# Kernel optimization log

Measured on AMD Instinct MI355X. Metric: run time of the kernel, lower is better.

Reference implementation:

```python
import jax, jax.numpy as jnp
import numpy as np

EPS = 1e-5


def _bn(x, g, b):
    # BatchNorm1d in training mode: batch mean, biased variance, eps=1e-5
    m = jnp.mean(x, axis=0)
    v = jnp.var(x, axis=0)
    return (x - m) * jax.lax.rsqrt(v + EPS) * g + b


def setup_inputs() -> dict:
    key = jax.random.key(0)
    ks = jax.random.split(key, 16)
    B, N, F, H = 4096, 128, 4, 32
    w = lambda k, o, i: jax.random.normal(k, (o, i), jnp.float32) * 0.3
    d = {
        'u': jax.random.normal(ks[0], (B, N, F), jnp.float32),
        'mask': jnp.ones((B * N, 1), jnp.int32),
        # MLPphi params
        'p_bn1_g': jnp.ones((F,), jnp.float32), 'p_bn1_b': jnp.zeros((F,), jnp.float32), 'p_w1': w(ks[1], H, F),
        'p_bn2_g': jnp.ones((H,), jnp.float32), 'p_bn2_b': jnp.zeros((H,), jnp.float32), 'p_w2': w(ks[2], H, H),
        'p_bn3_g': jnp.ones((H,), jnp.float32), 'p_bn3_b': jnp.zeros((H,), jnp.float32), 'p_w3': w(ks[3], H, H),
        # MLPomega params
        'o_bn1_g': jnp.ones((F,), jnp.float32), 'o_bn1_b': jnp.zeros((F,), jnp.float32), 'o_w1': w(ks[4], H, F),
        'o_bn2_g': jnp.ones((H,), jnp.float32), 'o_bn2_b': jnp.zeros((H,), jnp.float32), 'o_w2': w(ks[5], H, H),
        'o_bn3_g': jnp.ones((H,), jnp.float32), 'o_bn3_b': jnp.zeros((H,), jnp.float32), 'o_w3': w(ks[6], H, H),
        # MLPtheta params
        't_bn1_g': jnp.ones((H,), jnp.float32), 't_bn1_b': jnp.zeros((H,), jnp.float32), 't_w1': w(ks[7], H, H),
        't_bn2_g': jnp.ones((H,), jnp.float32), 't_bn2_b': jnp.zeros((H,), jnp.float32), 't_w2': w(ks[8], H, H),
        't_bn3_g': jnp.ones((H,), jnp.float32), 't_bn3_b': jnp.zeros((H,), jnp.float32), 't_w3': w(ks[9], H, H),
        't_bn4_g': jnp.ones((H,), jnp.float32), 't_bn4_b': jnp.zeros((H,), jnp.float32),
        't_w4': w(ks[10], 1, H), 't_b4': jnp.zeros((1,), jnp.float32),
    }
    return d


def _forward(u, mask,
             p_bn1_g, p_bn1_b, p_w1, p_bn2_g, p_bn2_b, p_w2, p_bn3_g, p_bn3_b, p_w3,
             o_bn1_g, o_bn1_b, o_w1, o_bn2_g, o_bn2_b, o_w2, o_bn3_g, o_bn3_b, o_w3,
             t_bn1_g, t_bn1_b, t_w1, t_bn2_g, t_bn2_b, t_w2, t_bn3_g, t_bn3_b, t_w3,
             t_bn4_g, t_bn4_b, t_w4, t_b4):
    B, N, F = u.shape
    H = p_w1.shape[0]
    u_flat = u.reshape(-1, F)  # (B*N, F)

    # MLPphi: three BN+Linear(no bias)+Tanh blocks with residual adds (dropout=identity in eval)
    o1 = jnp.tanh(_bn(u_flat, p_bn1_g, p_bn1_b) @ p_w1.T)
    o2 = jnp.tanh(_bn(o1, p_bn2_g, p_bn2_b) @ p_w2.T)
    o3 = jnp.tanh(_bn(o1 + o2, p_bn3_g, p_bn3_b) @ p_w3.T)
    x_main = (o1 + o2 + o3).reshape(B, N, H)

    # MLPomega: BN+Linear+Tanh x2, BN+Linear, softmax over hidden dim (dim=1 of flat), then masked_fill
    a = jnp.tanh(_bn(u_flat, o_bn1_g, o_bn1_b) @ o_w1.T)
    a = jnp.tanh(_bn(a, o_bn2_g, o_bn2_b) @ o_w2.T)
    a = _bn(a, o_bn3_g, o_bn3_b) @ o_w3.T
    a = jax.nn.softmax(a, axis=1)
    a = jnp.where(mask == 0, -jnp.inf, a)
    x_attn = a.reshape(B, N, H)

    # attention pooling over neighbors
    x = jnp.sum(x_main * x_attn, axis=1)  # (B, H)

    x = jnp.tanh(_bn(x, t_bn1_g, t_bn1_b) @ t_w1.T)
    x = jnp.tanh(_bn(x, t_bn2_g, t_bn2_b) @ t_w2.T)
    x = jnp.tanh(_bn(x, t_bn3_g, t_bn3_b) @ t_w3.T)
    x = _bn(x, t_bn4_g, t_bn4_b) @ t_w4.T + t_b4
    return x


def reference(u, mask,
              p_bn1_g, p_bn1_b, p_w1, p_bn2_g, p_bn2_b, p_w2, p_bn3_g, p_bn3_b, p_w3,
              o_bn1_g, o_bn1_b, o_w1, o_bn2_g, o_bn2_b, o_w2, o_bn3_g, o_bn3_b, o_w3,
              t_bn1_g, t_bn1_b, t_w1, t_bn2_g, t_bn2_b, t_w2, t_bn3_g, t_bn3_b, t_w3,
              t_bn4_g, t_bn4_b, t_w4, t_b4):
    return _forward(u, mask,
                    p_bn1_g, p_bn1_b, p_w1, p_bn2_g, p_bn2_b, p_w2, p_bn3_g, p_bn3_b, p_w3,
                    o_bn1_g, o_bn1_b, o_w1, o_bn2_g, o_bn2_b, o_w2, o_bn3_g, o_bn3_b, o_w3,
                    t_bn1_g, t_bn1_b, t_w1, t_bn2_g, t_bn2_b, t_w2, t_bn3_g, t_bn3_b, t_w3,
                    t_bn4_g, t_bn4_b, t_w4, t_b4)
```

## Files before the change

### kernel.cpp

```cpp
#include <hip/hip_runtime.h>

typedef unsigned int u32;
typedef unsigned short u16;
typedef __attribute__((ext_vector_type(8))) _Float16 half8;
typedef __attribute__((ext_vector_type(4))) float f32x4;

#define ROWS  524288
#define BROWS 4096
#define EPS   1e-5f

#define S_U   0
#define S_O1  8
#define S_A1  72
#define S_O12 136
#define S_A2  200
#define S_X   264
#define S_X1  328
#define S_X2  392
#define S_X3  456
#define SHARD 1024
#define NSH   64

#define XSTR 40

// ... 195 lines not shown

#define KIND_TANH          0
#define KIND_TANHRES       2
#define KIND_TANHRES_ATREG 3
template<int KIND>
__device__ __forceinline__ void mfma_layer(u16* X, const u16* Wt, const float* Cb,
                                           int L, int wv, int lane, const u32* at_pk)
{
  int ln15 = lane & 15, quad = lane >> 4;
  half8 w0 = *(const half8*)&Wt[(L*32 + ln15     )*XSTR + quad*8];
  half8 w1 = *(const half8*)&Wt[(L*32 + ln15 + 16)*XSTR + quad*8];
  float bias0[4], bias1[4];
#pragma unroll
  for (int reg=0;reg<4;++reg){
    bias0[reg] = Cb[L*32 +      quad*4 + reg];
    bias1[reg] = Cb[L*32 + 16 + quad*4 + reg];
  }
  int rowbase = wv*64;
#pragma unroll
  for (int Mt=0; Mt<4; ++Mt){
    int s = rowbase + Mt*16 + ln15;
    half8 bfr = *(const half8*)&X[s*XSTR + quad*8];
    f32x4 c0 = {0.f,0.f,0.f,0.f}, c1 = {0.f,0.f,0.f,0.f};
    c0 = __builtin_amdgcn_mfma_f32_16x16x32_f16(w0, bfr, c0, 0,0,0);
    c1 = __builtin_amdgcn_mfma_f32_16x16x32_f16(w1, bfr, c1, 0,0,0);
    float o0[4], o1v[4];
    if (KIND == KIND_TANHRES || KIND == KIND_TANHRES_ATREG){
      unpk4(*(const uint2*)&X[s*XSTR +      quad*4], o0);
      unpk4(*(const uint2*)&X[s*XSTR + 16 + quad*4], o1v);
    }
    float a0v[4], a1v[4];
    if (KIND == KIND_TANHRES_ATREG){
      a0v[0]=lo16(at_pk[Mt*4+0]); a0v[1]=hi16(at_pk[Mt*4+0]);
      a0v[2]=lo16(at_pk[Mt*4+1]); a0v[3]=hi16(at_pk[Mt*4+1]);
      a1v[0]=lo16(at_pk[Mt*4+2]); a1v[1]=hi16(at_pk[Mt*4+2]);
      a1v[2]=lo16(at_pk[Mt*4+3]); a1v[3]=hi16(at_pk[Mt*4+3]);
    }
    float v0[4], v1[4];
#pragma unroll
    for (int reg=0;reg<4;++reg){
      float a = c0[reg] + bias0[reg];
      float b = c1[reg] + bias1[reg];
      if (KIND == KIND_TANH){ a = tanh_fast(a); b = tanh_fast(b); }
      else if (KIND == KIND_TANHRES){ a = o0[reg] + tanh_fast(a); b = o1v[reg] + tanh_fast(b); }
      else if (KIND == KIND_TANHRES_ATREG){
        a = (o0[reg] + tanh_fast(a)) * a0v[reg];
        b = (o1v[reg] + tanh_fast(b)) * a1v[reg];
      }
      v0[reg] = a; v1[reg] = b;
    }
    uint2 w0o, w1o;
    w0o.x = pack2h(v0[0], v0[1]); w0o.y = pack2h(v0[2], v0[3]);
    w1o.x = pack2h(v1[0], v1[1]); w1o.y = pack2h(v1[2], v1[3]);
    *(uint2*)&X[s*XSTR +      quad*4] = w0o;
    *(uint2*)&X[s*XSTR + 16 + quad*4] = w1o;
  }
}

__device__ __forceinline__ void emit_stats(float* s8, float* q8, int tid, int wv,
    int quad, int ln15, float* scr , float* __restrict__ S, int offS, int shard)
{
#pragma unroll
  for (int i=0;i<8;++i){ s8[i]=red16(s8[i]); q8[i]=red16(q8[i]); }
  __syncthreads();
  if (ln15 == 0){
#pragma unroll
    for (int rg=0; rg<4; ++rg){
      int cl = quad*4+rg, ch = 16+quad*4+rg;
      scr[wv*64 + cl]       = s8[rg];
      scr[wv*64 + ch]       = s8[4+rg];
      scr[256 + wv*64 + cl] = q8[rg];
      scr[256 + wv*64 + ch] = q8[4+rg];
    }
  }
  __syncthreads();
  if (tid < 64){
    int j = tid & 31, isq = tid >> 5;
    const float* src = scr + isq*256;
    float tot = src[j] + src[64+j] + src[128+j] + src[192+j];
    atomicAdd(&S[shard*SHARD + offS + isq*32 + j], tot);
  }
}

__device__ __forceinline__ void mfma_logits_softmax_r(const half8* fa,
    const u16* Wt, const float* Cb, int L, int lane,
    const int* __restrict__ mask, int maskbase, u32* at_pk)
{
  int ln15 = lane & 15, quad = lane >> 4;
  half8 w0 = *(const half8*)&Wt[(L*32 + ln15     )*XSTR + quad*8];
  half8 w1 = *(const half8*)&Wt[(L*32 + ln15 + 16)*XSTR + quad*8];
  float bias0[4], bias1[4];
#pragma unroll
  for (int reg=0;reg<4;++reg){
    bias0[reg] = Cb[L*32 +      quad*4 + reg];
    bias1[reg] = Cb[L*32 + 16 + quad*4 + reg];
  }
#pragma unroll
  for (int Mt=0; Mt<4; ++Mt){
    f32x4 c0 = {0.f,0.f,0.f,0.f}, c1 = {0.f,0.f,0.f,0.f};
    c0 = __builtin_amdgcn_mfma_f32_16x16x32_f16(w0, fa[Mt], c0, 0,0,0);
    c1 = __builtin_amdgcn_mfma_f32_16x16x32_f16(w1, fa[Mt], c1, 0,0,0);
    float l0[4], l1[4];
#pragma unroll
    for (int reg=0;reg<4;++reg){ l0[reg] = c0[reg]+bias0[reg]; l1[reg] = c1[reg]+bias1[reg]; }
    float mx = l0[0];
#pragma unroll
    for (int reg=1;reg<4;++reg) mx = fmaxf(mx, l0[reg]);
#pragma unroll
    for (int reg=0;reg<4;++reg) mx = fmaxf(mx, l1[reg]);
    mx = fmaxf(mx, __shfl_xor(mx, 16));
    mx = fmaxf(mx, __shfl_xor(mx, 32));
    float sum = 0.f;
#pragma unroll
    for (int reg=0;reg<4;++reg){ l0[reg] = __expf(l0[reg]-mx); sum += l0[reg]; }
#pragma unroll
    for (int reg=0;reg<4;++reg){ l1[reg] = __expf(l1[reg]-mx); sum += l1[reg]; }
    sum += __shfl_xor(sum, 16);
    sum += __shfl_xor(sum, 32);
    float inv = __builtin_amdgcn_rcpf(sum);
    bool mz = (mask[maskbase + Mt*16 + ln15] == 0);
#pragma unroll
    for (int reg=0;reg<4;++reg){
      l0[reg] *= inv; l1[reg] *= inv;
      if (mz){ l0[reg] = -__builtin_inff(); l1[reg] = -__builtin_inff(); }
    }
    at_pk[Mt*4+0] = pack2h(l0[0], l0[1]);
    at_pk[Mt*4+1] = pack2h(l0[2], l0[3]);
    at_pk[Mt*4+2] = pack2h(l1[0], l1[1]);
    at_pk[Mt*4+3] = pack2h(l1[2], l1[3]);
  }
}

__device__ __forceinline__ void mfma_pool_r(const half8* fo, const uint2* r0, const uint2* r1,
    const u16* Wt, const float* Cb, int L, int lane, const u32* at_pk, float* ps)
{
  int ln15 = lane & 15, quad = lane >> 4;
  half8 w0 = *(const half8*)&Wt[(L*32 + ln15     )*XSTR + quad*8];
  half8 w1 = *(const half8*)&Wt[(L*32 + ln15 + 16)*XSTR + quad*8];
  float bias0[4], bias1[4];
#pragma unroll
  for (int reg=0;reg<4;++reg){
    bias0[reg] = Cb[L*32 +      quad*4 + reg];
    bias1[reg] = Cb[L*32 + 16 + quad*4 + reg];
  }
#pragma unroll
  for (int i=0;i<8;++i) ps[i]=0.f;
#pragma unroll
  for (int Mt=0; Mt<4; ++Mt){
    f32x4 c0 = {0.f,0.f,0.f,0.f}, c1 = {0.f,0.f,0.f,0.f};
    c0 = __builtin_amdgcn_mfma_f32_16x16x32_f16(w0, fo[Mt], c0, 0,0,0);
    c1 = __builtin_amdgcn_mfma_f32_16x16x32_f16(w1, fo[Mt], c1, 0,0,0);
    float o0[4], o1v[4];
    unpk4(r0[Mt], o0); unpk4(r1[Mt], o1v);
    float a0v[4], a1v[4];
    a0v[0]=lo16(at_pk[Mt*4+0]); a0v[1]=hi16(at_pk[Mt*4+0]);
    a0v[2]=lo16(at_pk[Mt*4+1]); a0v[3]=hi16(at_pk[Mt*4+1]);
    a1v[0]=lo16(at_pk[Mt*4+2]); a1v[1]=hi16(at_pk[Mt*4+2]);
    a1v[2]=lo16(at_pk[Mt*4+3]); a1v[3]=hi16(at_pk[Mt*4+3]);
#pragma unroll
    for (int reg=0;reg<4;++reg){
      float a = (o0[reg]  + tanh_fast(c0[reg]+bias0[reg])) * a0v[reg];
      float b = (o1v[reg] + tanh_fast(c1[reg]+bias1[reg])) * a1v[reg];
      ps[reg]   += a;
      ps[4+reg] += b;
    }
  }
}

__device__ __forceinline__ void reduce_f16(const u16* X, float* lds2,
                                           float* __restrict__ S, int offS, int shard)
{
  int tid = threadIdx.x;
  __syncthreads();
  {
    int j = tid & 31, seg = tid >> 5;
    float s=0.f, q=0.f;
#pragma unroll
    for (int q2=0;q2<32;++q2){
      float v = h2f(X[(seg*32+q2)*XSTR + j]);
      s += v; q = fmaf(v,v,q);
    }
    lds2[seg*32+j] = s;
    lds2[256 + seg*32+j] = q;
  }
  __syncthreads();
  if (tid < 64){
    int j = tid & 31; bool isq = tid >= 32;
    const float* src = lds2 + (isq?256:0);
    float tot=0.f;
#pragma unroll
    for (int sg=0;sg<8;++sg) tot += src[sg*32+j];
    atomicAdd(&S[shard*SHARD + offS + (isq?32:0) + j], tot);
  }
  __syncthreads();
}

__device__ __forceinline__ void reduce_f32(const float* Xs, float* lds2,
                                           float* __restrict__ S, int offS, int shard)
{
  int tid = threadIdx.x;
  __syncthreads();
  {
    int j = tid & 31, seg = tid >> 5;
    float s=0.f, q=0.f;
#pragma unroll
    for (int q2=0;q2<32;++q2){
      float v = Xs[(seg*32+q2)*33 + j];
      s += v; q = fmaf(v,v,q);
    }
    lds2[seg*32+j] = s;
    lds2[256 + seg*32+j] = q;
  }
  __syncthreads();
  if (tid < 64){
    int j = tid & 31; bool isq = tid >= 32;
    const float* src = lds2 + (isq?256:0);
    float tot=0.f;
#pragma unroll
    for (int sg=0;sg<8;++sg) tot += src[sg*32+j];
    atomicAdd(&S[shard*SHARD + offS + (isq?32:0) + j], tot);
  }
  __syncthreads();
}

template<bool F32, bool MAT>
__device__ __forceinline__ void pass1_body(const void* __restrict__ u,
    const void* pg1, const void* pb1, const void* pw1,
    const void* og1, const void* ob1, const void* ow1,
    float* __restrict__ S, u16* __restrict__ o1g, u16* __restrict__ a1g,
    u16* X, float* lds2, float* mr)
{
  int tid = threadIdx.x;
  int r = blockIdx.x*256 + tid;
  int shard = blockIdx.x & (NSH-1);
  float f[4], xn[4];
  load_u4<F32>(u,r,f);
  prep_u_par(S, mr, lds2, tid);

  bn_u_l<F32>(mr, pg1, pb1, f, xn);
  chain1_out<F32,MAT>(xn, pw1, X + tid*XSTR, o1g + (size_t)r*32);
  reduce_f16(X, lds2, S, S_O1, shard);

  bn_u_l<F32>(mr, og1, ob1, f, xn);
  chain1_out<F32,MAT>(xn, ow1, X + tid*XSTR, a1g + (size_t)r*32);
  reduce_f16(X, lds2, S, S_A1, shard);
}
template<bool MAT>
__global__ __launch_bounds__(256) void k_pass1(const void* __restrict__ u,
    const void* pg1, const void* pb1, const void* pw1,
    const void* og1, const void* ob1, const void* ow1,
    float* __restrict__ S, u16* o1g, u16* a1g){
  __shared__ u16 X[256*XSTR];
  __shared__ float lds2[512];
  __shared__ float mr[8];
  __shared__ int sf;
  int isf = detect_u((const u16*)u, threadIdx.x, &sf);
  if (isf) pass1_body<true ,MAT>(u,pg1,pb1,pw1,og1,ob1,ow1,S,o1g,a1g,X,lds2,mr);
  else     pass1_body<false,MAT>(u,pg1,pb1,pw1,og1,ob1,ow1,S,o1g,a1g,X,lds2,mr);
}

template<bool F32>
__device__ __forceinline__ void pass2m_body(
    const void* pg2, const void* pb2, const void* pw2,
    const void* og2, const void* ob2, const void* ow2,
    float* __restrict__ S, u16* __restrict__ o12g, u16* __restrict__ a2g,
    u16* Wt, float* Cb, float* lds2)
{
  int tid = threadIdx.x;
  int wv = tid >> 6, lane = tid & 63;
  int ln15 = lane & 15, quad = lane >> 4;
  int gbase = blockIdx.x*256;
  int shard = blockIdx.x & (NSH-1);

  half8 fo[4], fa[4]; uint2 r0[4], r1[4];
  int rowbase = wv*64;
#pragma unroll
  for (int Mt=0; Mt<4; ++Mt){
    size_t R = (size_t)(gbase + rowbase + Mt*16 + ln15);
    fo[Mt] = *(const half8*)&o12g[R*32 + quad*8];
    r0[Mt] = *(const uint2*)&o12g[R*32 +      quad*4];
    r1[Mt] = *(const uint2*)&o12g[R*32 + 16 + quad*4];
    fa[Mt] = *(const half8*)&a2g [R*32 + quad*8];
  }

  fold2<F32>(S, S_O1, S_A1, pg2,pb2,pw2, og2,ob2,ow2, Wt, Cb, lds2);

  float s8[8], q8[8];

  {
    half8 w0 = *(const half8*)&Wt[(ln15     )*XSTR + quad*8];
    half8 w1 = *(const half8*)&Wt[(ln15 + 16)*XSTR + quad*8];
    float bias0[4], bias1[4];
#pragma unroll
    for (int reg=0;reg<4;++reg){
      bias0[reg] = Cb[     quad*4 + reg];
      bias1[reg] = Cb[16 + quad*4 + reg];
    }
#pragma unroll
    for (int i=0;i<8;++i){ s8[i]=0.f; q8[i]=0.f; }
#pragma unroll
    for (int Mt=0; Mt<4; ++Mt){
      f32x4 c0 = {0.f,0.f,0.f,0.f}, c1 = {0.f,0.f,0.f,0.f};
      c0 = __builtin_amdgcn_mfma_f32_16x16x32_f16(w0, fo[Mt], c0, 0,0,0);
      c1 = __builtin_amdgcn_mfma_f32_16x16x32_f16(w1, fo[Mt], c1, 0,0,0);
      float o0[4], o1v[4];
      unpk4(r0[Mt], o0); unpk4(r1[Mt], o1v);
      float v0[4], v1[4];
#pragma unroll
      for (int reg=0;reg<4;++reg){
        float a = o0[reg]  + tanh_fast(c0[reg] + bias0[reg]);
        float b = o1v[reg] + tanh_fast(c1[reg] + bias1[reg]);
        s8[reg]   += a; q8[reg]   = fmaf(a,a,q8[reg]);
        s8[4+reg] += b; q8[4+reg] = fmaf(b,b,q8[4+reg]);
        v0[reg] = a; v1[reg] = b;
      }
      uint2 w0o, w1o;
      w0o.x = pack2h(v0[0], v0[1]); w0o.y = pack2h(v0[2], v0[3]);
      w1o.x = pack2h(v1[0], v1[1]); w1o.y = pack2h(v1[2], v1[3]);
      size_t R = (size_t)(gbase + rowbase + Mt*16 + ln15);
      *(uint2*)&o12g[R*32 +      quad*4] = w0o;
      *(uint2*)&o12g[R*32 + 16 + quad*4] = w1o;
    }
    emit_stats(s8, q8, tid, wv, quad, ln15, lds2, S, S_O12, shard);
  }

  {
    half8 w0 = *(const half8*)&Wt[(32 + ln15     )*XSTR + quad*8];
    half8 w1 = *(const half8*)&Wt[(32 + ln15 + 16)*XSTR + quad*8];
    float bias0[4], bias1[4];
#pragma unroll
    for (int reg=0;reg<4;++reg){
      bias0[reg] = Cb[32 +      quad*4 + reg];
      bias1[reg] = Cb[32 + 16 + quad*4 + reg];
    }
#pragma unroll
    for (int i=0;i<8;++i){ s8[i]=0.f; q8[i]=0.f; }
#pragma unroll
    for (int Mt=0; Mt<4; ++Mt){
      f32x4 c0 = {0.f,0.f,0.f,0.f}, c1 = {0.f,0.f,0.f,0.f};
      c0 = __builtin_amdgcn_mfma_f32_16x16x32_f16(w0, fa[Mt], c0, 0,0,0);
      c1 = __builtin_amdgcn_mfma_f32_16x16x32_f16(w1, fa[Mt], c1, 0,0,0);
      float v0[4], v1[4];
#pragma unroll
      for (int reg=0;reg<4;++reg){
        float a = tanh_fast(c0[reg] + bias0[reg]);
        float b = tanh_fast(c1[reg] + bias1[reg]);
        s8[reg]   += a; q8[reg]   = fmaf(a,a,q8[reg]);
        s8[4+reg] += b; q8[4+reg] = fmaf(b,b,q8[4+reg]);
        v0[reg] = a; v1[reg] = b;
      }
      uint2 w0o, w1o;
      w0o.x = pack2h(v0[0], v0[1]); w0o.y = pack2h(v0[2], v0[3]);
      w1o.x = pack2h(v1[0], v1[1]); w1o.y = pack2h(v1[2], v1[3]);
      size_t R = (size_t)(gbase + rowbase + Mt*16 + ln15);
      *(uint2*)&a2g[R*32 +      quad*4] = w0o;
      *(uint2*)&a2g[R*32 + 16 + quad*4] = w1o;
    }
    emit_stats(s8, q8, tid, wv, quad, ln15, lds2, S, S_A2, shard);
  }
}
__global__ __launch_bounds__(256) void k_pass2m(const void* __restrict__ u,
    const void* pg2, const void* pb2, const void* pw2,
    const void* og2, const void* ob2, const void* ow2,
    float* __restrict__ S, u16* o12g, u16* a2g){
  __shared__ u16 Wt[2*32*XSTR];
  __shared__ float Cb[64];
  __shared__ float lds2[512];
  __shared__ int sf;
  int isf = detect_u((const u16*)u, threadIdx.x, &sf);
  if (isf) pass2m_body<true >(pg2,pb2,pw2,og2,ob2,ow2,S,o12g,a2g,Wt,Cb,lds2);
  else     pass2m_body<false>(pg2,pb2,pw2,og2,ob2,ow2,S,o12g,a2g,Wt,Cb,lds2);
}

template<int KIND>
__device__ __forceinline__ void mfma_stat_l(const u16* X, const u16* Wt, const float* Cb,
    int L, int wv, int lane, float* s8, float* q8)
{
  int ln15 = lane & 15, quad = lane >> 4;
  half8 w0 = *(const half8*)&Wt[(L*32 + ln15     )*XSTR + quad*8];
  half8 w1 = *(const half8*)&Wt[(L*32 + ln15 + 16)*XSTR + quad*8];
  float bias0[4], bias1[4];
#pragma unroll
  for (int reg=0;reg<4;++reg){
    bias0[reg] = Cb[L*32 +      quad*4 + reg];
    bias1[reg] = Cb[L*32 + 16 + quad*4 + reg];
  }
#pragma unroll
  for (int i=0;i<8;++i){ s8[i]=0.f; q8[i]=0.f; }
  int rowbase = wv*64;
#pragma unroll
  for (int Mt=0; Mt<4; ++Mt){
    int s = rowbase + Mt*16 + ln15;
    half8 bfr = *(const half8*)&X[s*XSTR + quad*8];
    f32x4 c0 = {0.f,0.f,0.f,0.f}, c1 = {0.f,0.f,0.f,0.f};
    c0 = __builtin_amdgcn_mfma_f32_16x16x32_f16(w0, bfr, c0, 0,0,0);
    c1 = __builtin_amdgcn_mfma_f32_16x16x32_f16(w1, bfr, c1, 0,0,0);
    float o0[4], o1v[4];
    if (KIND == KIND_TANHRES){
      unpk4(*(const uint2*)&X[s*XSTR +      quad*4], o0);
      unpk4(*(const uint2*)&X[s*XSTR + 16 + quad*4], o1v);
    }
#pragma unroll
    for (int reg=0;reg<4;++reg){
      float a = c0[reg] + bias0[reg];
      float b = c1[reg] + bias1[reg];
      if (KIND == KIND_TANH){ a = tanh_fast(a); b = tanh_fast(b); }
      else { a = o0[reg] + tanh_fast(a); b = o1v[reg] + tanh_fast(b); }
      s8[reg]   += a; q8[reg]   = fmaf(a,a,q8[reg]);
      s8[4+reg] += b; q8[4+reg] = fmaf(b,b,q8[4+reg]);
    }
  }
}
template<bool F32>
__device__ __forceinline__ void pass2_body(const void* __restrict__ u,
    const void* pg1, const void* pb1, const void* pw1,
    const void* og1, const void* ob1, const void* ow1,
    const void* pg2, const void* pb2, const void* pw2,
    const void* og2, const void* ob2, const void* ow2,
    float* __restrict__ S,
    u16* X, u16* Wt, float* Cb, float* lds2, float* mr)
{
  int tid = threadIdx.x;
  int wv = tid >> 6, lane = tid & 63;
  int ln15 = lane & 15, quad = lane >> 4;
  int r = blockIdx.x*256 + tid;
  int shard = blockIdx.x & (NSH-1);
  float f[4], xn[4];
  load_u4<F32>(u,r,f);
  prep_u_par(S, mr, lds2, tid);
  fold2<F32>(S, S_O1, S_A1, pg2,pb2,pw2, og2,ob2,ow2, Wt, Cb, lds2);

  float s8[8], q8[8];

  bn_u_l<F32>(mr, pg1, pb1, f, xn);
  chain1_out<F32,false>(xn, pw1, X + tid*XSTR, 0);
  __syncthreads();
  mfma_stat_l<KIND_TANHRES>(X, Wt, Cb, 0, wv, lane, s8, q8);
  emit_stats(s8, q8, tid, wv, quad, ln15, lds2, S, S_O12, shard);

  bn_u_l<F32>(mr, og1, ob1, f, xn);
  chain1_out<F32,false>(xn, ow1, X + tid*XSTR, 0);
  __syncthreads();
  mfma_stat_l<KIND_TANH>(X, Wt, Cb, 1, wv, lane, s8, q8);
  emit_stats(s8, q8, tid, wv, quad, ln15, lds2, S, S_A2, shard);
}
__global__ __launch_bounds__(256) void k_pass2(const void* __restrict__ u,
    const void* pg1, const void* pb1, const void* pw1,
    const void* og1, const void* ob1, const void* ow1,
    const void* pg2, const void* pb2, const void* pw2,
    const void* og2, const void* ob2, const void* ow2,
    float* __restrict__ S){
  __shared__ u16 X[256*XSTR];
  __shared__ u16 Wt[2*32*XSTR];
  __shared__ float Cb[64];
  __shared__ float lds2[512];
  __shared__ float mr[8];
  __shared__ int sf;
  int isf = detect_u((const u16*)u, threadIdx.x, &sf);
  if (isf) pass2_body<true >(u,pg1,pb1,pw1,og1,ob1,ow1,pg2,pb2,pw2,og2,ob2,ow2,S,X,Wt,Cb,lds2,mr);
  else     pass2_body<false>(u,pg1,pb1,pw1,og1,ob1,ow1,pg2,pb2,pw2,og2,ob2,ow2,S,X,Wt,Cb,lds2,mr);
}

template<bool F32>
__device__ __forceinline__ void pass3m_body(const int* __restrict__ mask,
    const void* pg3, const void* pb3, const void* pw3,
    const void* og3, const void* ob3, const void* ow3,
    const u16* __restrict__ o12g, const u16* __restrict__ a2g,
    float* __restrict__ x, float* __restrict__ S,
    u16* Wt, float* Cb, float* lds2)
{
  int tid = threadIdx.x;
  int wv = tid >> 6, lane = tid & 63;
  int ln15 = lane & 15, quad = lane >> 4;
  int gbase = blockIdx.x*256;
  int rowbase = wv*64;

  half8 fo[4], fa[4]; uint2 r0[4], r1[4];
#pragma unroll
  for (int Mt=0; Mt<4; ++Mt){
    size_t R = (size_t)(gbase + rowbase + Mt*16 + ln15);
    fa[Mt] = *(const half8*)&a2g [R*32 + quad*8];
    fo[Mt] = *(const half8*)&o12g[R*32 + quad*8];
    r0[Mt] = *(const uint2*)&o12g[R*32 +      quad*4];
    r1[Mt] = *(const uint2*)&o12g[R*32 + 16 + quad*4];
  }

  fold2<F32>(S, S_A2, S_O12, og3,ob3,ow3, pg3,pb3,pw3, Wt, Cb, lds2);

  u32 at_pk[16];
  int maskbase = gbase + wv*64;
  mfma_logits_softmax_r(fa, Wt, Cb, 0, lane, mask, maskbase, at_pk);

  float ps[8];
  mfma_pool_r(fo, r0, r1, Wt, Cb, 1, lane, at_pk, ps);

#pragma unroll
  for (int i=0;i<8;++i) ps[i]=red16(ps[i]);
  __syncthreads();
  if (ln15 == 0){
#pragma unroll
    for (int rg=0; rg<4; ++rg){
      lds2[wv*32 + quad*4+rg]    = ps[rg];
      lds2[wv*32 + 16+quad*4+rg] = ps[4+rg];
    }
  }
  __syncthreads();
  if (tid < 64){
    int half = tid >> 5, j = tid & 31;
    float v = lds2[half*64 + j] + lds2[half*64 + 32 + j];
    x[(blockIdx.x*2 + half)*32 + j] = v;
    float* Sh = S + (blockIdx.x & (NSH-1))*SHARD;
    atomicAdd(&Sh[S_X+j], v);
    atomicAdd(&Sh[S_X+32+j], v*v);
  }
}
__global__ __launch_bounds__(256) void k_pass3m(const void* __restrict__ u, const int* __restrict__ mask,
    const void* pg3, const void* pb3, const void* pw3,
    const void* og3, const void* ob3, const void* ow3,
    const u16* o12g, const u16* a2g,
    float* __restrict__ x, float* __restrict__ S){
  __shared__ u16 Wt[2*32*XSTR];
  __shared__ float Cb[64];
  __shared__ float lds2[512];
  __shared__ int sf;
  int isf = detect_u((const u16*)u, threadIdx.x, &sf);
  if (isf) pass3m_body<true >(mask,pg3,pb3,pw3,og3,ob3,ow3,o12g,a2g,x,S,Wt,Cb,lds2);
  else     pass3m_body<false>(mask,pg3,pb3,pw3,og3,ob3,ow3,o12g,a2g,x,S,Wt,Cb,lds2);
}

template<bool F32>
__device__ __forceinline__ void fold4(const float* __restrict__ S,
    int off0,int off1,int off2,int off3,
    const void* g0,const void* b0,const void* W0,
    const void* g1,const void* b1,const void* W1,
    const void* g2,const void* b2,const void* W2,
    const void* g3,const void* b3,const void* W3,
    u16* Wt, float* Cb, float* scr)
{
  int tid = threadIdx.x;
  __shared__ float scr2[256];
  if (tid < 128){
    int L = tid>>5, k = tid&31;
    const void* g = (L==0)?g0:(L==1)?g1:(L==2)?g2:g3;
    const void* b = (L==0)?b0:(L==1)?b1:(L==2)?b2:b3;
    int off = (L==0)?off0:(L==1)?off1:(L==2)?off2:off3;
    float s=0.f, q=0.f;
#pragma unroll
    for (int sh=0; sh<NSH; ++sh){
      s += S[sh*SHARD + off + k];
      q += S[sh*SHARD + off + 32 + k];
    }
    float m    = s*(1.0f/ROWS);
    float var  = q*(1.0f/ROWS) - m*m;
    float rstd = rsqrtf(var+EPS);
    float sc = rdp<F32>(g,k)*rstd;
    scr[tid]  = sc;
    scr2[tid] = rdp<F32>(b,k) - m*sc;
  }
  __syncthreads();
  if (tid < 128){
    int L = tid>>5, j = tid&31;
    const void* W = (L==0)?W0:(L==1)?W1:(L==2)?W2:W3;
    float c = 0.f;
#pragma unroll
    for (int k=0;k<32;++k){
      float Wv = rdp<F32>(W, j*32+k);
      Wt[(L*32+j)*XSTR + k] = f2h(Wv * scr[(L<<5)|k]);
      c += Wv * scr2[(L<<5)|k];
    }
    Cb[L*32+j] = c;
  }
  __syncthreads();
}

template<bool F32>
__device__ __forceinline__ void pass3_body(const void* __restrict__ u, const int* __restrict__ mask,
    const void* pg1, const void* pb1, const void* pw1,
    const void* og1, const void* ob1, const void* ow1,
    const void* pg2, const void* pb2, const void* pw2,
    const void* og2, const void* ob2, const void* ow2,
    const void* pg3, const void* pb3, const void* pw3,
    const void* og3, const void* ob3, const void* ow3,
    float* __restrict__ x, float* __restrict__ S,
    u16* X, u16* Wt, float* Cb, float* red2, float* mr)
{
  int tid = threadIdx.x;
  int wv = tid >> 6, lane = tid & 63;
  int r = blockIdx.x*256 + tid;
  float f[4], xn[4];
  load_u4<F32>(u,r,f);
  prep_u_par(S, mr, red2, tid);
  fold4<F32>(S, S_A1, S_A2, S_O1, S_O12,
             og2,ob2,ow2, og3,ob3,ow3, pg2,pb2,pw2, pg3,pb3,pw3,
             Wt, Cb, red2);

  u32 at_pk[16];
// ... 163 lines not shown
    const float* __restrict__ xin, float* __restrict__ xout,
    float* __restrict__ S, int off_in, int off_out,
    const void* g, const void* b, const void* W){
  __shared__ float lds[256*33];
  __shared__ float lds2[512];
  __shared__ int sf;
  int isf = detect_u((const u16*)u, threadIdx.x, &sf);
  if (isf) theta_L_body<true , NSH_IN>(xin, xout, S, off_in, off_out, g, b, W, lds, lds2);
  else     theta_L_body<false, NSH_IN>(xin, xout, S, off_in, off_out, g, b, W, lds, lds2);
}

template<bool F32>
__device__ __forceinline__ void theta_fin_body(const float* __restrict__ xin,
    float* __restrict__ S,
    const void* g4, const void* b4, const void* w4, const void* bb4,
    void* out, float* lds, float* lds2)
{
  int tid = threadIdx.x, blk = blockIdx.x;
  int r = blk*256 + tid;
  const float4* xr = (const float4*)&xin[(size_t)r*32];
  float4 t0 = xr[0], t1 = xr[1], t2 = xr[2], t3 = xr[3];
  float4 t4 = xr[4], t5 = xr[5], t6 = xr[6], t7 = xr[7];
  theta_gather<16>(S, S_X3, lds, lds2, tid);
  float vv[32];
  vv[0]=t0.x; vv[1]=t0.y; vv[2]=t0.z; vv[3]=t0.w;
  vv[4]=t1.x; vv[5]=t1.y; vv[6]=t1.z; vv[7]=t1.w;
  vv[8]=t2.x; vv[9]=t2.y; vv[10]=t2.z; vv[11]=t2.w;
  vv[12]=t3.x; vv[13]=t3.y; vv[14]=t3.z; vv[15]=t3.w;
  vv[16]=t4.x; vv[17]=t4.y; vv[18]=t4.z; vv[19]=t4.w;
  vv[20]=t5.x; vv[21]=t5.y; vv[22]=t5.z; vv[23]=t5.w;
  vv[24]=t6.x; vv[25]=t6.y; vv[26]=t6.z; vv[27]=t6.w;
  vv[28]=t7.x; vv[29]=t7.y; vv[30]=t7.z; vv[31]=t7.w;
  float acc = rdp<F32>(bb4, 0);
#pragma unroll
  for (int k=0;k<32;++k){
    float xnv = (vv[k] - lds2[k]) * (rdp<F32>(g4,k)*lds2[32+k]) + rdp<F32>(b4,k);
    acc = fmaf(rdp<F32>(w4,k), xnv, acc);
  }
  if (F32) ((float*)out)[r] = acc;
  else     ((u16*)out)[r]  = f2b(acc);
}
__global__ __launch_bounds__(256) void k_theta_fin(const void* __restrict__ u,
    const float* __restrict__ xin, float* __restrict__ S,
    const void* g4, const void* b4, const void* w4, const void* bb4,
    void* out){
  __shared__ float lds[256];
  __shared__ float lds2[512];
  __shared__ int sf;
  int isf = detect_u((const u16*)u, threadIdx.x, &sf);
  if (isf) theta_fin_body<true >(xin, S, g4, b4, w4, bb4, out, lds, lds2);
  else     theta_fin_body<false>(xin, S, g4, b4, w4, bb4, out, lds, lds2);
}

extern "C" void kernel_launch(void* const* d_in, const int* in_sizes, int n_in,
                              void* d_out, int out_size, void* d_ws, size_t ws_size,
                              hipStream_t stream)
{
  const void* u    = d_in[0];
  const int*  mask = (const int*)d_in[1];
  const void *pg1=d_in[2],  *pb1=d_in[3],  *pw1=d_in[4];
  const void *pg2=d_in[5],  *pb2=d_in[6],  *pw2=d_in[7];
  const void *pg3=d_in[8],  *pb3=d_in[9],  *pw3=d_in[10];
  const void *og1=d_in[11], *ob1=d_in[12], *ow1=d_in[13];
  const void *og2=d_in[14], *ob2=d_in[15], *ow2=d_in[16];
  const void *og3=d_in[17], *ob3=d_in[18], *ow3=d_in[19];
  const void *tg1=d_in[20], *tb1=d_in[21], *tw1=d_in[22];
  const void *tg2=d_in[23], *tb2=d_in[24], *tw2=d_in[25];
  const void *tg3=d_in[26], *tb3=d_in[27], *tw3=d_in[28];
  const void *tg4=d_in[29], *tb4=d_in[30], *tw4=d_in[31], *tbb4=d_in[32];

  char* ws = (char*)d_ws;
  float* S    = (float*)(ws + 4096);
  float* x    = (float*)(ws + 524288);
  float* xb   = (float*)(ws + 1048576);

  const size_t MB = 1024*1024;
  u16* o12g = (u16*)(ws + 8*MB);
  u16* a2g  = (u16*)(ws + 40*MB);
  bool MAT = ws_size >= 73*MB;

  (void)hipMemsetAsync(ws, 0, 4096 + NSH*SHARD*4, stream);
  k_stats_u<<<1024, 256, 0, stream>>>(u, S);
  if (MAT){
    k_pass1<true ><<<2048, 256, 0, stream>>>(u, pg1,pb1,pw1, og1,ob1,ow1, S, o12g, a2g);
    k_pass2m<<<2048, 256, 0, stream>>>(u, pg2,pb2,pw2, og2,ob2,ow2, S, o12g, a2g);
    k_pass3m<<<2048, 256, 0, stream>>>(u, mask, pg3,pb3,pw3, og3,ob3,ow3, o12g, a2g, x, S);
  } else {
    k_pass1<false><<<2048, 256, 0, stream>>>(u, pg1,pb1,pw1, og1,ob1,ow1, S, o12g, a2g);
    k_pass2<<<2048, 256, 0, stream>>>(u, pg1,pb1,pw1, og1,ob1,ow1,
                                      pg2,pb2,pw2, og2,ob2,ow2, S);
    k_pass3<<<2048, 256, 0, stream>>>(u, mask, pg1,pb1,pw1, og1,ob1,ow1,
                                      pg2,pb2,pw2, og2,ob2,ow2,
                                      pg3,pb3,pw3, og3,ob3,ow3, x, S);
  }
  k_theta_L<64><<<16, 256, 0, stream>>>(u, x,  xb, S, S_X,  S_X1, tg1, tb1, tw1);
  k_theta_L<16><<<16, 256, 0, stream>>>(u, xb, x,  S, S_X1, S_X2, tg2, tb2, tw2);
  k_theta_L<16><<<16, 256, 0, stream>>>(u, x,  xb, S, S_X2, S_X3, tg3, tb3, tw3);
  k_theta_fin<<<16, 256, 0, stream>>>(u, xb, S, tg4, tb4, tw4, tbb4, d_out);
}
```

Baseline: 330.2 us.

## Process four row tiles per block with double-buffered loads in passes

The three main passes now launch a quarter of the blocks, and each block loops over four 256-row groups. Passes 2m and 3m double-buffer the half8 MFMA operand loads, prefetching the next group while computing the current one. The per-block fold of BN statistics into weights and the weight and bias register loads are amortised over four times as many rows, and BN stat emission in pass 2 happens once per block. The trade-offs are higher register pressure from the doubled buffers and only 512 blocks, which may reduce occupancy and latency hiding.

```diff
diff --git a/kernel.cpp b/kernel.cpp
--- a/kernel.cpp
+++ b/kernel.cpp
@@ -301,91 +301,6 @@
   }
 }
 
-__device__ __forceinline__ void mfma_logits_softmax_r(const half8* fa,
-    const u16* Wt, const float* Cb, int L, int lane,
-    const int* __restrict__ mask, int maskbase, u32* at_pk)
-{
-  int ln15 = lane & 15, quad = lane >> 4;
-  half8 w0 = *(const half8*)&Wt[(L*32 + ln15     )*XSTR + quad*8];
-  half8 w1 = *(const half8*)&Wt[(L*32 + ln15 + 16)*XSTR + quad*8];
-  float bias0[4], bias1[4];
-#pragma unroll
-  for (int reg=0;reg<4;++reg){
-    bias0[reg] = Cb[L*32 +      quad*4 + reg];
-    bias1[reg] = Cb[L*32 + 16 + quad*4 + reg];
-  }
-#pragma unroll
-  for (int Mt=0; Mt<4; ++Mt){
-    f32x4 c0 = {0.f,0.f,0.f,0.f}, c1 = {0.f,0.f,0.f,0.f};
-    c0 = __builtin_amdgcn_mfma_f32_16x16x32_f16(w0, fa[Mt], c0, 0,0,0);
-    c1 = __builtin_amdgcn_mfma_f32_16x16x32_f16(w1, fa[Mt], c1, 0,0,0);
-    float l0[4], l1[4];
-#pragma unroll
-    for (int reg=0;reg<4;++reg){ l0[reg] = c0[reg]+bias0[reg]; l1[reg] = c1[reg]+bias1[reg]; }
-    float mx = l0[0];
-#pragma unroll
-    for (int reg=1;reg<4;++reg) mx = fmaxf(mx, l0[reg]);
-#pragma unroll
-    for (int reg=0;reg<4;++reg) mx = fmaxf(mx, l1[reg]);
-    mx = fmaxf(mx, __shfl_xor(mx, 16));
-    mx = fmaxf(mx, __shfl_xor(mx, 32));
-    float sum = 0.f;
-#pragma unroll
-    for (int reg=0;reg<4;++reg){ l0[reg] = __expf(l0[reg]-mx); sum += l0[reg]; }
-#pragma unroll
-    for (int reg=0;reg<4;++reg){ l1[reg] = __expf(l1[reg]-mx); sum += l1[reg]; }
-    sum += __shfl_xor(sum, 16);
-    sum += __shfl_xor(sum, 32);
-    float inv = __builtin_amdgcn_rcpf(sum);
-    bool mz = (mask[maskbase + Mt*16 + ln15] == 0);
-#pragma unroll
-    for (int reg=0;reg<4;++reg){
-      l0[reg] *= inv; l1[reg] *= inv;
-      if (mz){ l0[reg] = -__builtin_inff(); l1[reg] = -__builtin_inff(); }
-    }
-    at_pk[Mt*4+0] = pack2h(l0[0], l0[1]);
-    at_pk[Mt*4+1] = pack2h(l0[2], l0[3]);
-    at_pk[Mt*4+2] = pack2h(l1[0], l1[1]);
-    at_pk[Mt*4+3] = pack2h(l1[2], l1[3]);
-  }
-}
-
-__device__ __forceinline__ void mfma_pool_r(const half8* fo, const uint2* r0, const uint2* r1,
-    const u16* Wt, const float* Cb, int L, int lane, const u32* at_pk, float* ps)
-{
-  int ln15 = lane & 15, quad = lane >> 4;
-  half8 w0 = *(const half8*)&Wt[(L*32 + ln15     )*XSTR + quad*8];
-  half8 w1 = *(const half8*)&Wt[(L*32 + ln15 + 16)*XSTR + quad*8];
-  float bias0[4], bias1[4];
-#pragma unroll
-  for (int reg=0;reg<4;++reg){
-    bias0[reg] = Cb[L*32 +      quad*4 + reg];
-    bias1[reg] = Cb[L*32 + 16 + quad*4 + reg];
-  }
-#pragma unroll
-  for (int i=0;i<8;++i) ps[i]=0.f;
-#pragma unroll
-  for (int Mt=0; Mt<4; ++Mt){
-    f32x4 c0 = {0.f,0.f,0.f,0.f}, c1 = {0.f,0.f,0.f,0.f};
-    c0 = __builtin_amdgcn_mfma_f32_16x16x32_f16(w0, fo[Mt], c0, 0,0,0);
-    c1 = __builtin_amdgcn_mfma_f32_16x16x32_f16(w1, fo[Mt], c1, 0,0,0);
-    float o0[4], o1v[4];
-    unpk4(r0[Mt], o0); unpk4(r1[Mt], o1v);
-    float a0v[4], a1v[4];
-    a0v[0]=lo16(at_pk[Mt*4+0]); a0v[1]=hi16(at_pk[Mt*4+0]);
-    a0v[2]=lo16(at_pk[Mt*4+1]); a0v[3]=hi16(at_pk[Mt*4+1]);
-    a1v[0]=lo16(at_pk[Mt*4+2]); a1v[1]=hi16(at_pk[Mt*4+2]);
-    a1v[2]=lo16(at_pk[Mt*4+3]); a1v[3]=hi16(at_pk[Mt*4+3]);
-#pragma unroll
-    for (int reg=0;reg<4;++reg){
-      float a = (o0[reg]  + tanh_fast(c0[reg]+bias0[reg])) * a0v[reg];
-      float b = (o1v[reg] + tanh_fast(c1[reg]+bias1[reg])) * a1v[reg];
-      ps[reg]   += a;
-      ps[4+reg] += b;
-    }
-  }
-}
-
 __device__ __forceinline__ void reduce_f16(const u16* X, float* lds2,
                                            float* __restrict__ S, int offS, int shard)
 {
@@ -450,19 +365,25 @@
     u16* X, float* lds2, float* mr)
 {
   int tid = threadIdx.x;
-  int r = blockIdx.x*256 + tid;
+  int base = blockIdx.x*1024;
   int shard = blockIdx.x & (NSH-1);
-  float f[4], xn[4];
-  load_u4<F32>(u,r,f);
+  float f[4][4];
+#pragma unroll
+  for (int g=0; g<4; ++g) load_u4<F32>(u, base + g*256 + tid, f[g]);
   prep_u_par(S, mr, lds2, tid);
 
-  bn_u_l<F32>(mr, pg1, pb1, f, xn);
-  chain1_out<F32,MAT>(xn, pw1, X + tid*XSTR, o1g + (size_t)r*32);
-  reduce_f16(X, lds2, S, S_O1, shard);
-
-  bn_u_l<F32>(mr, og1, ob1, f, xn);
-  chain1_out<F32,MAT>(xn, ow1, X + tid*XSTR, a1g + (size_t)r*32);
-  reduce_f16(X, lds2, S, S_A1, shard);
+#pragma unroll
+  for (int g=0; g<4; ++g){
+    int r = base + g*256 + tid;
+    float xn[4];
+    bn_u_l<F32>(mr, pg1, pb1, f[g], xn);
+    chain1_out<F32,MAT>(xn, pw1, X + tid*XSTR, o1g + (size_t)r*32);
+    reduce_f16(X, lds2, S, S_O1, shard);
+
+    bn_u_l<F32>(mr, og1, ob1, f[g], xn);
+    chain1_out<F32,MAT>(xn, ow1, X + tid*XSTR, a1g + (size_t)r*32);
+    reduce_f16(X, lds2, S, S_A1, shard);
+  }
 }
 template<bool MAT>
 __global__ __launch_bounds__(256) void k_pass1(const void* __restrict__ u,
@@ -478,6 +399,12 @@
   else     pass1_body<false,MAT>(u,pg1,pb1,pw1,og1,ob1,ow1,S,o1g,a1g,X,lds2,mr);
 }
 
+#define P2_LOADM(BUF, G, MT) { \
+  size_t R = (size_t)(gbase + (G)*256 + rowbase + (MT)*16 + ln15); \
+  fo[BUF][MT] = *(const half8*)&o12g[R*32 + quad*8]; \
+  fa[BUF][MT] = *(const half8*)&a2g [R*32 + quad*8]; }
+#define P2_LOAD(BUF, G) P2_LOADM(BUF,G,0) P2_LOADM(BUF,G,1) P2_LOADM(BUF,G,2) P2_LOADM(BUF,G,3)
+
 template<bool F32>
 __device__ __forceinline__ void pass2m_body(
     const void* pg2, const void* pb2, const void* pw2,
@@ -488,95 +415,88 @@
   int tid = threadIdx.x;
   int wv = tid >> 6, lane = tid & 63;
   int ln15 = lane & 15, quad = lane >> 4;
-  int gbase = blockIdx.x*256;
+  int gbase = blockIdx.x*1024;
   int shard = blockIdx.x & (NSH-1);
-
-  half8 fo[4], fa[4]; uint2 r0[4], r1[4];
   int rowbase = wv*64;
-#pragma unroll
-  for (int Mt=0; Mt<4; ++Mt){
-    size_t R = (size_t)(gbase + rowbase + Mt*16 + ln15);
-    fo[Mt] = *(const half8*)&o12g[R*32 + quad*8];
-    r0[Mt] = *(const uint2*)&o12g[R*32 +      quad*4];
-    r1[Mt] = *(const uint2*)&o12g[R*32 + 16 + quad*4];
-    fa[Mt] = *(const half8*)&a2g [R*32 + quad*8];
-  }
+
+  half8 fo[2][4], fa[2][4];
+  P2_LOAD(0, 0)
 
   fold2<F32>(S, S_O1, S_A1, pg2,pb2,pw2, og2,ob2,ow2, Wt, Cb, lds2);
 
-  float s8[8], q8[8];
-
-  {
-    half8 w0 = *(const half8*)&Wt[(ln15     )*XSTR + quad*8];
-    half8 w1 = *(const half8*)&Wt[(ln15 + 16)*XSTR + quad*8];
-    float bias0[4], bias1[4];
-#pragma unroll
-    for (int reg=0;reg<4;++reg){
-      bias0[reg] = Cb[     quad*4 + reg];
-      bias1[reg] = Cb[16 + quad*4 + reg];
-    }
-#pragma unroll
-    for (int i=0;i<8;++i){ s8[i]=0.f; q8[i]=0.f; }
+  half8 w0o = *(const half8*)&Wt[(ln15     )*XSTR + quad*8];
+  half8 w1o = *(const half8*)&Wt[(ln15 + 16)*XSTR + quad*8];
+  half8 w0a = *(const half8*)&Wt[(32 + ln15     )*XSTR + quad*8];
+  half8 w1a = *(const half8*)&Wt[(32 + ln15 + 16)*XSTR + quad*8];
+  float b0o[4], b1o[4], b0a[4], b1a[4];
+#pragma unroll
+  for (int reg=0;reg<4;++reg){
+    b0o[reg] = Cb[     quad*4 + reg]; b1o[reg] = Cb[16 + quad*4 + reg];
+    b0a[reg] = Cb[32 + quad*4 + reg]; b1a[reg] = Cb[48 + quad*4 + reg];
+  }
+
+  float s8o[8], q8o[8], s8a[8], q8a[8];
+#pragma unroll
+  for (int i=0;i<8;++i){ s8o[i]=0.f; q8o[i]=0.f; s8a[i]=0.f; q8a[i]=0.f; }
+
+#pragma unroll
+  for (int g=0; g<4; ++g){
+    const int buf = g & 1;
+    if (g < 3){ P2_LOAD(buf^1, g+1) }
+    uint2 r0[4], r1[4];
 #pragma unroll
     for (int Mt=0; Mt<4; ++Mt){
-      f32x4 c0 = {0.f,0.f,0.f,0.f}, c1 = {0.f,0.f,0.f,0.f};
-      c0 = __builtin_amdgcn_mfma_f32_16x16x32_f16(w0, fo[Mt], c0, 0,0,0);
-      c1 = __builtin_amdgcn_mfma_f32_16x16x32_f16(w1, fo[Mt], c1, 0,0,0);
-      float o0[4], o1v[4];
-      unpk4(r0[Mt], o0); unpk4(r1[Mt], o1v);
-      float v0[4], v1[4];
-#pragma unroll
-      for (int reg=0;reg<4;++reg){
-        float a = o0[reg]  + tanh_fast(c0[reg] + bias0[reg]);
-        float b = o1v[reg] + tanh_fast(c1[reg] + bias1[reg]);
-        s8[reg]   += a; q8[reg]   = fmaf(a,a,q8[reg]);
-        s8[4+reg] += b; q8[4+reg] = fmaf(b,b,q8[4+reg]);
-        v0[reg] = a; v1[reg] = b;
+      size_t R = (size_t)(gbase + g*256 + rowbase + Mt*16 + ln15);
+      r0[Mt] = *(const uint2*)&o12g[R*32 +      quad*4];
+      r1[Mt] = *(const uint2*)&o12g[R*32 + 16 + quad*4];
+    }
+#pragma unroll
+    for (int Mt=0; Mt<4; ++Mt){
+      size_t R = (size_t)(gbase + g*256 + rowbase + Mt*16 + ln15);
+      {
+        f32x4 c0 = {0.f,0.f,0.f,0.f}, c1 = {0.f,0.f,0.f,0.f};
+        c0 = __builtin_amdgcn_mfma_f32_16x16x32_f16(w0o, fo[buf][Mt], c0, 0,0,0);
+        c1 = __builtin_amdgcn_mfma_f32_16x16x32_f16(w1o, fo[buf][Mt], c1, 0,0,0);
+        float o0[4], o1v[4];
+        unpk4(r0[Mt], o0); unpk4(r1[Mt], o1v);
+        float v0[4], v1[4];
+#pragma unroll
+        for (int reg=0;reg<4;++reg){
+          float a = o0[reg]  + tanh_fast(c0[reg] + b0o[reg]);
+          float b = o1v[reg] + tanh_fast(c1[reg] + b1o[reg]);
+          s8o[reg]   += a; q8o[reg]   = fmaf(a,a,q8o[reg]);
+          s8o[4+reg] += b; q8o[4+reg] = fmaf(b,b,q8o[4+reg]);
+          v0[reg] = a; v1[reg] = b;
+        }
+        uint2 wA, wB;
+        wA.x = pack2h(v0[0], v0[1]); wA.y = pack2h(v0[2], v0[3]);
+        wB.x = pack2h(v1[0], v1[1]); wB.y = pack2h(v1[2], v1[3]);
+        *(uint2*)&o12g[R*32 +      quad*4] = wA;
+        *(uint2*)&o12g[R*32 + 16 + quad*4] = wB;
       }
-      uint2 w0o, w1o;
-      w0o.x = pack2h(v0[0], v0[1]); w0o.y = pack2h(v0[2], v0[3]);
-      w1o.x = pack2h(v1[0], v1[1]); w1o.y = pack2h(v1[2], v1[3]);
-      size_t R = (size_t)(gbase + rowbase + Mt*16 + ln15);
-      *(uint2*)&o12g[R*32 +      quad*4] = w0o;
-      *(uint2*)&o12g[R*32 + 16 + quad*4] = w1o;
-    }
-    emit_stats(s8, q8, tid, wv, quad, ln15, lds2, S, S_O12, shard);
-  }
-
-  {
-    half8 w0 = *(const half8*)&Wt[(32 + ln15     )*XSTR + quad*8];
-    half8 w1 = *(const half8*)&Wt[(32 + ln15 + 16)*XSTR + quad*8];
-    float bias0[4], bias1[4];
-#pragma unroll
-    for (int reg=0;reg<4;++reg){
-      bias0[reg] = Cb[32 +      quad*4 + reg];
-      bias1[reg] = Cb[32 + 16 + quad*4 + reg];
-    }
-#pragma unroll
-    for (int i=0;i<8;++i){ s8[i]=0.f; q8[i]=0.f; }
-#pragma unroll
-    for (int Mt=0; Mt<4; ++Mt){
-      f32x4 c0 = {0.f,0.f,0.f,0.f}, c1 = {0.f,0.f,0.f,0.f};
-      c0 = __builtin_amdgcn_mfma_f32_16x16x32_f16(w0, fa[Mt], c0, 0,0,0);
-      c1 = __builtin_amdgcn_mfma_f32_16x16x32_f16(w1, fa[Mt], c1, 0,0,0);
-      float v0[4], v1[4];
-#pragma unroll
-      for (int reg=0;reg<4;++reg){
-        float a = tanh_fast(c0[reg] + bias0[reg]);
-        float b = tanh_fast(c1[reg] + bias1[reg]);
-        s8[reg]   += a; q8[reg]   = fmaf(a,a,q8[reg]);
-        s8[4+reg] += b; q8[4+reg] = fmaf(b,b,q8[4+reg]);
-        v0[reg] = a; v1[reg] = b;
+      {
+        f32x4 c0 = {0.f,0.f,0.f,0.f}, c1 = {0.f,0.f,0.f,0.f};
+        c0 = __builtin_amdgcn_mfma_f32_16x16x32_f16(w0a, fa[buf][Mt], c0, 0,0,0);
+        c1 = __builtin_amdgcn_mfma_f32_16x16x32_f16(w1a, fa[buf][Mt], c1, 0,0,0);
+        float v0[4], v1[4];
+#pragma unroll
+        for (int reg=0;reg<4;++reg){
+          float a = tanh_fast(c0[reg] + b0a[reg]);
+          float b = tanh_fast(c1[reg] + b1a[reg]);
+          s8a[reg]   += a; q8a[reg]   = fmaf(a,a,q8a[reg]);
+          s8a[4+reg] += b; q8a[4+reg] = fmaf(b,b,q8a[4+reg]);
+          v0[reg] = a; v1[reg] = b;
+        }
+        uint2 wA, wB;
+        wA.x = pack2h(v0[0], v0[1]); wA.y = pack2h(v0[2], v0[3]);
+        wB.x = pack2h(v1[0], v1[1]); wB.y = pack2h(v1[2], v1[3]);
+        *(uint2*)&a2g[R*32 +      quad*4] = wA;
+        *(uint2*)&a2g[R*32 + 16 + quad*4] = wB;
       }
-      uint2 w0o, w1o;
-      w0o.x = pack2h(v0[0], v0[1]); w0o.y = pack2h(v0[2], v0[3]);
-      w1o.x = pack2h(v1[0], v1[1]); w1o.y = pack2h(v1[2], v1[3]);
-      size_t R = (size_t)(gbase + rowbase + Mt*16 + ln15);
-      *(uint2*)&a2g[R*32 +      quad*4] = w0o;
-      *(uint2*)&a2g[R*32 + 16 + quad*4] = w1o;
-    }
-    emit_stats(s8, q8, tid, wv, quad, ln15, lds2, S, S_A2, shard);
-  }
+    }
+  }
+  emit_stats(s8o, q8o, tid, wv, quad, ln15, lds2, S, S_O12, shard);
+  emit_stats(s8a, q8a, tid, wv, quad, ln15, lds2, S, S_A2, shard);
 }
 __global__ __launch_bounds__(256) void k_pass2m(const void* __restrict__ u,
     const void* pg2, const void* pb2, const void* pw2,
@@ -680,6 +600,12 @@
   else     pass2_body<false>(u,pg1,pb1,pw1,og1,ob1,ow1,pg2,pb2,pw2,og2,ob2,ow2,S,X,Wt,Cb,lds2,mr);
 }
 
+#define P3_LOADM(BUF, G, MT) { \
+  size_t R = (size_t)(gbase + (G)*256 + rowbase + (MT)*16 + ln15); \
+  fa[BUF][MT] = *(const half8*)&a2g [R*32 + quad*8]; \
+  fo[BUF][MT] = *(const half8*)&o12g[R*32 + quad*8]; }
+#define P3_LOAD(BUF, G) P3_LOADM(BUF,G,0) P3_LOADM(BUF,G,1) P3_LOADM(BUF,G,2) P3_LOADM(BUF,G,3)
+
 template<bool F32>
 __device__ __forceinline__ void pass3m_body(const int* __restrict__ mask,
     const void* pg3, const void* pb3, const void* pw3,
@@ -691,46 +617,115 @@
   int tid = threadIdx.x;
   int wv = tid >> 6, lane = tid & 63;
   int ln15 = lane & 15, quad = lane >> 4;
-  int gbase = blockIdx.x*256;
+  int gbase = blockIdx.x*1024;
+  int shard = blockIdx.x & (NSH-1);
   int rowbase = wv*64;
 
-  half8 fo[4], fa[4]; uint2 r0[4], r1[4];
-#pragma unroll
-  for (int Mt=0; Mt<4; ++Mt){
-    size_t R = (size_t)(gbase + rowbase + Mt*16 + ln15);
-    fa[Mt] = *(const half8*)&a2g [R*32 + quad*8];
-    fo[Mt] = *(const half8*)&o12g[R*32 + quad*8];
-    r0[Mt] = *(const uint2*)&o12g[R*32 +      quad*4];
-    r1[Mt] = *(const uint2*)&o12g[R*32 + 16 + quad*4];
-  }
+  half8 fa[2][4], fo[2][4];
+  P3_LOAD(0, 0)
 
   fold2<F32>(S, S_A2, S_O12, og3,ob3,ow3, pg3,pb3,pw3, Wt, Cb, lds2);
 
-  u32 at_pk[16];
-  int maskbase = gbase + wv*64;
-  mfma_logits_softmax_r(fa, Wt, Cb, 0, lane, mask, maskbase, at_pk);
-
-  float ps[8];
-  mfma_pool_r(fo, r0, r1, Wt, Cb, 1, lane, at_pk, ps);
-
-#pragma unroll
-  for (int i=0;i<8;++i) ps[i]=red16(ps[i]);
-  __syncthreads();
-  if (ln15 == 0){
-#pragma unroll
-    for (int rg=0; rg<4; ++rg){
-      lds2[wv*32 + quad*4+rg]    = ps[rg];
-      lds2[wv*32 + 16+quad*4+rg] = ps[4+rg];
-    }
-  }
-  __syncthreads();
-  if (tid < 64){
-    int half = tid >> 5, j = tid & 31;
-    float v = lds2[half*64 + j] + lds2[half*64 + 32 + j];
-    x[(blockIdx.x*2 + half)*32 + j] = v;
-    float* Sh = S + (blockIdx.x & (NSH-1))*SHARD;
-    atomicAdd(&Sh[S_X+j], v);
-    atomicAdd(&Sh[S_X+32+j], v*v);
+  half8 w0s = *(const half8*)&Wt[(ln15     )*XSTR + quad*8];
+  half8 w1s = *(const half8*)&Wt[(ln15 + 16)*XSTR + quad*8];
+  half8 w0p = *(const half8*)&Wt[(32 + ln15     )*XSTR + quad*8];
+  half8 w1p = *(const half8*)&Wt[(32 + ln15 + 16)*XSTR + quad*8];
+  float b0s[4], b1s[4], b0p[4], b1p[4];
+#pragma unroll
+  for (int reg=0;reg<4;++reg){
+    b0s[reg] = Cb[     quad*4 + reg]; b1s[reg] = Cb[16 + quad*4 + reg];
+    b0p[reg] = Cb[32 + quad*4 + reg]; b1p[reg] = Cb[48 + quad*4 + reg];
+  }
+
+#pragma unroll
+  for (int g=0; g<4; ++g){
+    const int buf = g & 1;
+    if (g < 3){ P3_LOAD(buf^1, g+1) }
+    uint2 r0[4], r1[4];
+#pragma unroll
+    for (int Mt=0; Mt<4; ++Mt){
+      size_t R = (size_t)(gbase + g*256 + rowbase + Mt*16 + ln15);
+      r0[Mt] = *(const uint2*)&o12g[R*32 +      quad*4];
+      r1[Mt] = *(const uint2*)&o12g[R*32 + 16 + quad*4];
+    }
+    int maskbase = gbase + g*256 + wv*64;
+    u32 at_pk[16];
+#pragma unroll
+    for (int Mt=0; Mt<4; ++Mt){
+      f32x4 c0 = {0.f,0.f,0.f,0.f}, c1 = {0.f,0.f,0.f,0.f};
+      c0 = __builtin_amdgcn_mfma_f32_16x16x32_f16(w0s, fa[buf][Mt], c0, 0,0,0);
+      c1 = __builtin_amdgcn_mfma_f32_16x16x32_f16(w1s, fa[buf][Mt], c1, 0,0,0);
+      float l0[4], l1[4];
+#pragma unroll
+      for (int reg=0;reg<4;++reg){ l0[reg] = c0[reg]+b0s[reg]; l1[reg] = c1[reg]+b1s[reg]; }
+      float mx = l0[0];
+#pragma unroll
+      for (int reg=1;reg<4;++reg) mx = fmaxf(mx, l0[reg]);
+#pragma unroll
+      for (int reg=0;reg<4;++reg) mx = fmaxf(mx, l1[reg]);
+      mx = fmaxf(mx, __shfl_xor(mx, 16));
+      mx = fmaxf(mx, __shfl_xor(mx, 32));
+      float sum = 0.f;
+#pragma unroll
+      for (int reg=0;reg<4;++reg){ l0[reg] = __expf(l0[reg]-mx); sum += l0[reg]; }
+#pragma unroll
+      for (int reg=0;reg<4;++reg){ l1[reg] = __expf(l1[reg]-mx); sum += l1[reg]; }
+      sum += __shfl_xor(sum, 16);
+      sum += __shfl_xor(sum, 32);
+      float inv = __builtin_amdgcn_rcpf(sum);
+      bool mz = (mask[maskbase + Mt*16 + ln15] == 0);
+#pragma unroll
+      for (int reg=0;reg<4;++reg){
+        l0[reg] *= inv; l1[reg] *= inv;
+        if (mz){ l0[reg] = -__builtin_inff(); l1[reg] = -__builtin_inff(); }
+      }
+      at_pk[Mt*4+0] = pack2h(l0[0], l0[1]);
+      at_pk[Mt*4+1] = pack2h(l0[2], l0[3]);
+      at_pk[Mt*4+2] = pack2h(l1[0], l1[1]);
+      at_pk[Mt*4+3] = pack2h(l1[2], l1[3]);
+    }
+    float ps[8];
+#pragma unroll
+    for (int i=0;i<8;++i) ps[i]=0.f;
+#pragma unroll
+    for (int Mt=0; Mt<4; ++Mt){
+      f32x4 c0 = {0.f,0.f,0.f,0.f}, c1 = {0.f,0.f,0.f,0.f};
+      c0 = __builtin_amdgcn_mfma_f32_16x16x32_f16(w0p, fo[buf][Mt], c0, 0,0,0);
+      c1 = __builtin_amdgcn_mfma_f32_16x16x32_f16(w1p, fo[buf][Mt], c1, 0,0,0);
+      float o0[4], o1v[4];
+      unpk4(r0[Mt], o0); unpk4(r1[Mt], o1v);
+      float a0v[4], a1v[4];
+      a0v[0]=lo16(at_pk[Mt*4+0]); a0v[1]=hi16(at_pk[Mt*4+0]);
+      a0v[2]=lo16(at_pk[Mt*4+1]); a0v[3]=hi16(at_pk[Mt*4+1]);
+      a1v[0]=lo16(at_pk[Mt*4+2]); a1v[1]=hi16(at_pk[Mt*4+2]);
+      a1v[2]=lo16(at_pk[Mt*4+3]); a1v[3]=hi16(at_pk[Mt*4+3]);
+#pragma unroll
+      for (int reg=0;reg<4;++reg){
+        float a = (o0[reg]  + tanh_fast(c0[reg]+b0p[reg])) * a0v[reg];
+        float b = (o1v[reg] + tanh_fast(c1[reg]+b1p[reg])) * a1v[reg];
+        ps[reg]   += a;
+        ps[4+reg] += b;
+      }
+    }
+#pragma unroll
+    for (int i=0;i<8;++i) ps[i]=red16(ps[i]);
+    __syncthreads();
+    if (ln15 == 0){
+#pragma unroll
+      for (int rg=0; rg<4; ++rg){
+        lds2[wv*32 + quad*4+rg]    = ps[rg];
+        lds2[wv*32 + 16+quad*4+rg] = ps[4+rg];
+      }
+    }
+    __syncthreads();
+    if (tid < 64){
+      int half = tid >> 5, j = tid & 31;
+      float v = lds2[half*64 + j] + lds2[half*64 + 32 + j];
+      x[((size_t)blockIdx.x*8 + g*2 + half)*32 + j] = v;
+      float* Sh = S + shard*SHARD;
+      atomicAdd(&Sh[S_X+j], v);
+      atomicAdd(&Sh[S_X+32+j], v*v);
+    }
   }
 }
 __global__ __launch_bounds__(256) void k_pass3m(const void* __restrict__ u, const int* __restrict__ mask,
@@ -1060,11 +1055,11 @@
   (void)hipMemsetAsync(ws, 0, 4096 + NSH*SHARD*4, stream);
   k_stats_u<<<1024, 256, 0, stream>>>(u, S);
   if (MAT){
-    k_pass1<true ><<<2048, 256, 0, stream>>>(u, pg1,pb1,pw1, og1,ob1,ow1, S, o12g, a2g);
-    k_pass2m<<<2048, 256, 0, stream>>>(u, pg2,pb2,pw2, og2,ob2,ow2, S, o12g, a2g);
-    k_pass3m<<<2048, 256, 0, stream>>>(u, mask, pg3,pb3,pw3, og3,ob3,ow3, o12g, a2g, x, S);
+    k_pass1<true ><<<512, 256, 0, stream>>>(u, pg1,pb1,pw1, og1,ob1,ow1, S, o12g, a2g);
+    k_pass2m<<<512, 256, 0, stream>>>(u, pg2,pb2,pw2, og2,ob2,ow2, S, o12g, a2g);
+    k_pass3m<<<512, 256, 0, stream>>>(u, mask, pg3,pb3,pw3, og3,ob3,ow3, o12g, a2g, x, S);
   } else {
-    k_pass1<false><<<2048, 256, 0, stream>>>(u, pg1,pb1,pw1, og1,ob1,ow1, S, o12g, a2g);
+    k_pass1<false><<<512, 256, 0, stream>>>(u, pg1,pb1,pw1, og1,ob1,ow1, S, o12g, a2g);
     k_pass2<<<2048, 256, 0, stream>>>(u, pg1,pb1,pw1, og1,ob1,ow1,
                                       pg2,pb2,pw2, og2,ob2,ow2, S);
     k_pass3<<<2048, 256, 0, stream>>>(u, mask, pg1,pb1,pw1, og1,ob1,ow1,
```

New measurement: 308.7 us, median of 2. -6.5%, faster.
